# Optimization experiments

Measured on AMD Instinct MI355X. Metric: run time of the kernel, lower is better.

The kernel has to match this reference:

```python
import jax, jax.numpy as jnp
import numpy as np

B, T, QD, AD = 64, 4096, 1024, 256
SCORE_MASK_VALUE = -1e30


def setup_inputs() -> dict:
    key = jax.random.key(0)
    k1, k2, k3, k4, k5 = jax.random.split(key, 5)
    query = jax.random.normal(k1, (B, QD), dtype=jnp.float32)
    processed_memory = jax.random.normal(k2, (B, T, AD), dtype=jnp.float32)
    mask = jax.random.randint(k3, (B, T), 0, 2).astype(bool)
    Wq = jax.random.normal(k4, (AD, QD), dtype=jnp.float32) * (1.0 / np.sqrt(QD))
    v = jax.random.normal(k5, (AD,), dtype=jnp.float32) * (1.0 / np.sqrt(AD))
    return {"query": query, "processed_memory": processed_memory, "mask": mask, "Wq": Wq, "v": v}


def reference(query, processed_memory, mask, Wq, v):
    # processed_query: (B, AD) -> broadcast over time
    processed_query = query @ Wq.T                      # (B, AD)
    hidden = jnp.tanh(processed_query[:, None, :] + processed_memory)  # (B, T, AD)
    energies = jnp.einsum('btd,d->bt', hidden, v)       # (B, T)
    energies = jnp.where(mask, SCORE_MASK_VALUE, energies)
    alignment = jax.nn.softmax(energies, axis=1)        # (B, T)
    return alignment
```

## Files before the change

kernel.cpp:

```cpp
#include <hip/hip_runtime.h>
#include <math.h>

#define B_  64
#define T_  4096
#define QD_ 1024
#define AD_ 256
#define MASKVAL (-1e30f)

__global__ __launch_bounds__(256) void pq_kernel(const float* __restrict__ query,
                                                 const float* __restrict__ Wq,
                                                 float* __restrict__ pq) {
    __shared__ float qs[QD_];
    const int b   = blockIdx.x;
    const int tid = threadIdx.x;
    ((float4*)qs)[tid] = ((const float4*)(query + (size_t)b * QD_))[tid];
    __syncthreads();

    const int d = tid;
    const float4* w4 = (const float4*)(Wq + (size_t)d * QD_);
    float sum = 0.f;
#pragma unroll 8
    for (int k = 0; k < QD_ / 4; ++k) {
        const float4 w = w4[k];
        const float4 q = ((const float4*)qs)[k];
        sum += q.x * w.x + q.y * w.y + q.z * w.z + q.w * w.w;
    }
    pq[(size_t)b * AD_ + d] = sum;
}

__global__ __launch_bounds__(256) void energy_kernel(const float* __restrict__ pm,
                                                     const int*   __restrict__ mask,
                                                     const float* __restrict__ pq,
                                                     const float* __restrict__ v,
                                                     float* __restrict__ energies) {
    const int wave = threadIdx.x >> 6;
    const int lane = threadIdx.x & 63;
    const size_t idx = (size_t)blockIdx.x * 4 + wave;
    const int b = (int)(idx >> 12);

    if (mask[idx]) {
        if (lane == 0) energies[idx] = MASKVAL;
        return;
    }

    const float4 m  = ((const float4*)pm)[idx * (AD_ / 4) + lane];
    const float4 q  = ((const float4*)(pq + (size_t)b * AD_))[lane];
    const float4 vv = ((const float4*)v)[lane];

    float e = tanhf(q.x + m.x) * vv.x
            + tanhf(q.y + m.y) * vv.y
            + tanhf(q.z + m.z) * vv.z
            + tanhf(q.w + m.w) * vv.w;

#pragma unroll
    for (int off = 32; off > 0; off >>= 1)
        e += __shfl_xor(e, off, 64);

    if (lane == 0) energies[idx] = e;
}

__global__ __launch_bounds__(256) void softmax_kernel(const float* __restrict__ energies,
                                                      float* __restrict__ out) {
    const int b    = blockIdx.x;
    const int tid  = threadIdx.x;
    const int wave = tid >> 6;
    const int lane = tid & 63;
    __shared__ float redmax[4];
    __shared__ float redsum[4];

    const float4* e4 = (const float4*)(energies + (size_t)b * T_);
    float4 vals[4];
    float mx = -INFINITY;
#pragma unroll
    for (int i = 0; i < 4; ++i) {
        vals[i] = e4[i * 256 + tid];
        mx = fmaxf(mx, fmaxf(fmaxf(vals[i].x, vals[i].y), fmaxf(vals[i].z, vals[i].w)));
    }
#pragma unroll
    for (int off = 32; off > 0; off >>= 1)
        mx = fmaxf(mx, __shfl_xor(mx, off, 64));
    if (lane == 0) redmax[wave] = mx;
    __syncthreads();
    mx = fmaxf(fmaxf(redmax[0], redmax[1]), fmaxf(redmax[2], redmax[3]));

    float s = 0.f;
#pragma unroll
    for (int i = 0; i < 4; ++i) {
        vals[i].x = expf(vals[i].x - mx);
        vals[i].y = expf(vals[i].y - mx);
        vals[i].z = expf(vals[i].z - mx);
        vals[i].w = expf(vals[i].w - mx);
        s += vals[i].x + vals[i].y + vals[i].z + vals[i].w;
    }
#pragma unroll
    for (int off = 32; off > 0; off >>= 1)
        s += __shfl_xor(s, off, 64);
    if (lane == 0) redsum[wave] = s;
    __syncthreads();
    s = redsum[0] + redsum[1] + redsum[2] + redsum[3];

    const float inv = 1.f / s;
    float4* o4 = (float4*)(out + (size_t)b * T_);
#pragma unroll
    for (int i = 0; i < 4; ++i) {
        vals[i].x *= inv; vals[i].y *= inv; vals[i].z *= inv; vals[i].w *= inv;
        o4[i * 256 + tid] = vals[i];
    }
}

extern "C" void kernel_launch(void* const* d_in, const int* in_sizes, int n_in,
                              void* d_out, int out_size, void* d_ws, size_t ws_size,
                              hipStream_t stream) {
    const float* query = (const float*)d_in[0];
    const float* pm    = (const float*)d_in[1];
    const int*   mask  = (const int*)  d_in[2];
    const float* Wq    = (const float*)d_in[3];
    const float* v     = (const float*)d_in[4];
    float* out = (float*)d_out;

    float* pq       = (float*)d_ws;
    float* energies = pq + (size_t)B_ * AD_;

    pq_kernel<<<B_, 256, 0, stream>>>(query, Wq, pq);
    energy_kernel<<<(B_ * T_) / 4, 256, 0, stream>>>(pm, mask, pq, v, energies);
    softmax_kernel<<<B_, 256, 0, stream>>>(energies, out);
}
```

Measured before the change: 394.2 us.

## Parallelize pq per wave, batch four timesteps per wave, use fast tanh/exp

The query projection now gives one wavefront to each output element and reduces with shuffles. It launches many more blocks than the old 64-block kernel, where each thread walked an Wq row strided across lanes. The energy kernel handles four timesteps per wave, reads the mask as an int4 and skips masked rows, and swaps tanhf for an exp2/rcp approximation. Softmax moves to 512 threads and uses exp2. The fast tanh and exp trade a little accuracy for fewer instructions.

```diff
diff --git a/kernel.cpp b/kernel.cpp
--- a/kernel.cpp
+++ b/kernel.cpp
@@ -6,26 +6,36 @@
 #define QD_ 1024
 #define AD_ 256
 #define MASKVAL (-1e30f)
+#define LOG2E 1.44269504f
+
+__device__ __forceinline__ float tanh_fast(float x) {
+    float xc = fminf(fmaxf(x, -9.0f), 9.0f);
+    float e  = __builtin_amdgcn_exp2f(xc * (2.0f * LOG2E));
+    return (e - 1.0f) * __builtin_amdgcn_rcpf(e + 1.0f);
+}
 
 __global__ __launch_bounds__(256) void pq_kernel(const float* __restrict__ query,
                                                  const float* __restrict__ Wq,
                                                  float* __restrict__ pq) {
-    __shared__ float qs[QD_];
-    const int b   = blockIdx.x;
-    const int tid = threadIdx.x;
-    ((float4*)qs)[tid] = ((const float4*)(query + (size_t)b * QD_))[tid];
-    __syncthreads();
+    const int wave = threadIdx.x >> 6;
+    const int lane = threadIdx.x & 63;
+    const int w = blockIdx.x * 4 + wave;
+    const int b = w >> 8;
+    const int d = w & 255;
 
-    const int d = tid;
+    const float4* q4 = (const float4*)(query + (size_t)b * QD_);
     const float4* w4 = (const float4*)(Wq + (size_t)d * QD_);
     float sum = 0.f;
-#pragma unroll 8
-    for (int k = 0; k < QD_ / 4; ++k) {
-        const float4 w = w4[k];
-        const float4 q = ((const float4*)qs)[k];
-        sum += q.x * w.x + q.y * w.y + q.z * w.z + q.w * w.w;
+#pragma unroll
+    for (int j = 0; j < QD_ / 4 / 64; ++j) {
+        const float4 a = q4[j * 64 + lane];
+        const float4 c = w4[j * 64 + lane];
+        sum += a.x * c.x + a.y * c.y + a.z * c.z + a.w * c.w;
     }
-    pq[(size_t)b * AD_ + d] = sum;
+#pragma unroll
+    for (int off = 32; off > 0; off >>= 1)
+        sum += __shfl_xor(sum, off, 64);
+    if (lane == 0) pq[w] = sum;
 }
 
 __global__ __launch_bounds__(256) void energy_kernel(const float* __restrict__ pm,
@@ -35,77 +45,90 @@
                                                      float* __restrict__ energies) {
     const int wave = threadIdx.x >> 6;
     const int lane = threadIdx.x & 63;
-    const size_t idx = (size_t)blockIdx.x * 4 + wave;
-    const int b = (int)(idx >> 12);
+    const size_t grp = (size_t)blockIdx.x * 4 + wave;
+    const size_t t0  = grp * 4;
+    const int b = (int)(t0 >> 12);
 
-    if (mask[idx]) {
-        if (lane == 0) energies[idx] = MASKVAL;
-        return;
-    }
+    const int4 mk = ((const int4*)mask)[grp];
+    const int msk0 = __builtin_amdgcn_readfirstlane(mk.x);
+    const int msk1 = __builtin_amdgcn_readfirstlane(mk.y);
+    const int msk2 = __builtin_amdgcn_readfirstlane(mk.z);
+    const int msk3 = __builtin_amdgcn_readfirstlane(mk.w);
+    const int msk[4] = {msk0, msk1, msk2, msk3};
 
-    const float4 m  = ((const float4*)pm)[idx * (AD_ / 4) + lane];
     const float4 q  = ((const float4*)(pq + (size_t)b * AD_))[lane];
     const float4 vv = ((const float4*)v)[lane];
 
-    float e = tanhf(q.x + m.x) * vv.x
-            + tanhf(q.y + m.y) * vv.y
-            + tanhf(q.z + m.z) * vv.z
-            + tanhf(q.w + m.w) * vv.w;
+    const float4* pm4 = (const float4*)pm;
+    float4 m[4];
+#pragma unroll
+    for (int i = 0; i < 4; ++i)
+        if (!msk[i]) m[i] = pm4[(t0 + i) * (AD_ / 4) + lane];
 
+    float res[4];
 #pragma unroll
-    for (int off = 32; off > 0; off >>= 1)
-        e += __shfl_xor(e, off, 64);
-
-    if (lane == 0) energies[idx] = e;
+    for (int i = 0; i < 4; ++i) {
+        if (msk[i]) { res[i] = MASKVAL; continue; }
+        float e = tanh_fast(q.x + m[i].x) * vv.x
+                + tanh_fast(q.y + m[i].y) * vv.y
+                + tanh_fast(q.z + m[i].z) * vv.z
+                + tanh_fast(q.w + m[i].w) * vv.w;
+#pragma unroll
+        for (int off = 32; off > 0; off >>= 1)
+            e += __shfl_xor(e, off, 64);
+        res[i] = e;
+    }
+    if (lane == 0)
+        ((float4*)energies)[grp] = make_float4(res[0], res[1], res[2], res[3]);
 }
 
-__global__ __launch_bounds__(256) void softmax_kernel(const float* __restrict__ energies,
+__global__ __launch_bounds__(512) void softmax_kernel(const float* __restrict__ energies,
                                                       float* __restrict__ out) {
     const int b    = blockIdx.x;
     const int tid  = threadIdx.x;
     const int wave = tid >> 6;
     const int lane = tid & 63;
-    __shared__ float redmax[4];
-    __shared__ float redsum[4];
+    __shared__ float redmax[8];
+    __shared__ float redsum[8];
 
     const float4* e4 = (const float4*)(energies + (size_t)b * T_);
-    float4 vals[4];
-    float mx = -INFINITY;
-#pragma unroll
-    for (int i = 0; i < 4; ++i) {
-        vals[i] = e4[i * 256 + tid];
-        mx = fmaxf(mx, fmaxf(fmaxf(vals[i].x, vals[i].y), fmaxf(vals[i].z, vals[i].w)));
-    }
+    float4 v0 = e4[tid];
+    float4 v1 = e4[tid + 512];
+
+    float mx = fmaxf(fmaxf(fmaxf(v0.x, v0.y), fmaxf(v0.z, v0.w)),
+                     fmaxf(fmaxf(v1.x, v1.y), fmaxf(v1.z, v1.w)));
 #pragma unroll
     for (int off = 32; off > 0; off >>= 1)
         mx = fmaxf(mx, __shfl_xor(mx, off, 64));
     if (lane == 0) redmax[wave] = mx;
     __syncthreads();
-    mx = fmaxf(fmaxf(redmax[0], redmax[1]), fmaxf(redmax[2], redmax[3]));
+#pragma unroll
+    for (int i = 0; i < 8; ++i) mx = fmaxf(mx, redmax[i]);
 
-    float s = 0.f;
-#pragma unroll
-    for (int i = 0; i < 4; ++i) {
-        vals[i].x = expf(vals[i].x - mx);
-        vals[i].y = expf(vals[i].y - mx);
-        vals[i].z = expf(vals[i].z - mx);
-        vals[i].w = expf(vals[i].w - mx);
-        s += vals[i].x + vals[i].y + vals[i].z + vals[i].w;
-    }
+    v0.x = __builtin_amdgcn_exp2f((v0.x - mx) * LOG2E);
+    v0.y = __builtin_amdgcn_exp2f((v0.y - mx) * LOG2E);
+    v0.z = __builtin_amdgcn_exp2f((v0.z - mx) * LOG2E);
+    v0.w = __builtin_amdgcn_exp2f((v0.w - mx) * LOG2E);
+    v1.x = __builtin_amdgcn_exp2f((v1.x - mx) * LOG2E);
+    v1.y = __builtin_amdgcn_exp2f((v1.y - mx) * LOG2E);
+    v1.z = __builtin_amdgcn_exp2f((v1.z - mx) * LOG2E);
+    v1.w = __builtin_amdgcn_exp2f((v1.w - mx) * LOG2E);
+    float s = v0.x + v0.y + v0.z + v0.w + v1.x + v1.y + v1.z + v1.w;
 #pragma unroll
     for (int off = 32; off > 0; off >>= 1)
         s += __shfl_xor(s, off, 64);
     if (lane == 0) redsum[wave] = s;
     __syncthreads();
-    s = redsum[0] + redsum[1] + redsum[2] + redsum[3];
+    s = 0.f;
+#pragma unroll
+    for (int i = 0; i < 8; ++i) s += redsum[i];
 
     const float inv = 1.f / s;
     float4* o4 = (float4*)(out + (size_t)b * T_);
-#pragma unroll
-    for (int i = 0; i < 4; ++i) {
-        vals[i].x *= inv; vals[i].y *= inv; vals[i].z *= inv; vals[i].w *= inv;
-        o4[i * 256 + tid] = vals[i];
-    }
+    v0.x *= inv; v0.y *= inv; v0.z *= inv; v0.w *= inv;
+    v1.x *= inv; v1.y *= inv; v1.z *= inv; v1.w *= inv;
+    o4[tid]       = v0;
+    o4[tid + 512] = v1;
 }
 
 extern "C" void kernel_launch(void* const* d_in, const int* in_sizes, int n_in,
@@ -121,7 +144,7 @@
     float* pq       = (float*)d_ws;
     float* energies = pq + (size_t)B_ * AD_;
 
-    pq_kernel<<<B_, 256, 0, stream>>>(query, Wq, pq);
-    energy_kernel<<<(B_ * T_) / 4, 256, 0, stream>>>(pm, mask, pq, v, energies);
-    softmax_kernel<<<B_, 256, 0, stream>>>(energies, out);
+    pq_kernel<<<(B_ * AD_) / 4, 256, 0, stream>>>(query, Wq, pq);
+    energy_kernel<<<(B_ * T_) / 16, 256, 0, stream>>>(pm, mask, pq, v, energies);
+    softmax_kernel<<<B_, 512, 0, stream>>>(energies, out);
 }
```

After: 341.8 us. -13.3%, faster.
